# Performance work log

Hardware: AMD Instinct MI355X
Metric: run time of the kernel (lower is better)

Reference implementation:

```python
import jax, jax.numpy as jnp
import numpy as np

TAU = 0.1

def _conv(x, w, padding):
    return jax.lax.conv_general_dilated(
        x, w, window_strides=(1, 1), padding=padding,
        dimension_numbers=("NCHW", "OIHW", "NCHW"))


def _bilinear_border(img, gx, gy):
    # img: (H,W). gx,gy: (H,W) normalized coords in [-1,1].
    # Matches torch grid_sample(mode='bilinear', align_corners=True, padding_mode='border').
    H, W = img.shape
    px = jnp.clip((gx + 1.0) * 0.5 * (W - 1), 0.0, W - 1)  # border: clamp coord
    py = jnp.clip((gy + 1.0) * 0.5 * (H - 1), 0.0, H - 1)
    x0 = jnp.floor(px)
    y0 = jnp.floor(py)
    wx = px - x0
    wy = py - y0
    x0i = x0.astype(jnp.int32)
    y0i = y0.astype(jnp.int32)
    x1i = jnp.minimum(x0i + 1, W - 1)
    y1i = jnp.minimum(y0i + 1, H - 1)
    v00 = img[y0i, x0i]
    v01 = img[y0i, x1i]
    v10 = img[y1i, x0i]
    v11 = img[y1i, x1i]
    top = v00 * (1.0 - wx) + v01 * wx
    bot = v10 * (1.0 - wx) + v11 * wx
    return top * (1.0 - wy) + bot * wy

_sample = jax.vmap(_bilinear_border)  # over flattened B*C axis


def setup_inputs() -> dict:
    key = jax.random.key(0)
    k1, k2, k3, k4 = jax.random.split(key, 4)
    B, C, H, W = 8, 64, 192, 192
    SH = 8
    x = jax.random.normal(k1, (B, C, H, W), dtype=jnp.float32)
    # kaiming_normal * 0.1 scale on first conv
    w1 = jax.random.normal(k2, (SH, C, 3, 3), dtype=jnp.float32) * (np.sqrt(2.0 / (C * 9)) * 0.1)
    # original zero-inits w2; use small random values for a nontrivial reference
    w2 = jax.random.normal(k3, (4 * C, SH, 1, 1), dtype=jnp.float32) * 0.02
    b2 = jax.random.normal(k4, (4 * C,), dtype=jnp.float32) * 0.5
    log_scale = jnp.asarray(np.log(0.1), dtype=jnp.float32)
    return {"x": x, "w1": w1, "w2": w2, "b2": b2, "log_scale": log_scale}


def reference(x, w1, w2, b2, log_scale):
    B, C, H, W = x.shape
    h = jax.nn.gelu(_conv(x, w1, "SAME"), approximate=False)
    coeffs = _conv(h, w2, "VALID") + b2[None, :, None, None]  # (B,4C,H,W)
    coeffs = coeffs.reshape(B, C, 4, H, W)  # channel = c*4 + k, as in torch .view
    a = jax.nn.softplus(coeffs[:, :, 0])
    bx = coeffs[:, :, 1]
    by = coeffs[:, :, 2]
    c = jnp.clip(coeffs[:, :, 3], -5.0, 5.0)
    s = jnp.sqrt(a * TAU + 1e-8).reshape(B * C, H, W)
    dx = (bx * TAU).reshape(B * C, H, W)
    dy = (by * TAU).reshape(B * C, H, W)
    bgx = jnp.broadcast_to(jnp.linspace(-1.0, 1.0, W, dtype=x.dtype)[None, :], (H, W))[None]
    bgy = jnp.broadcast_to(jnp.linspace(-1.0, 1.0, H, dtype=x.dtype)[:, None], (H, W))[None]
    xf = x.reshape(B * C, H, W)
    u_px = _sample(xf, bgx + s + dx, bgy + dy)
    u_nx = _sample(xf, bgx - s + dx, bgy + dy)
    u_py = _sample(xf, bgx + dx, bgy + s + dy)
    u_ny = _sample(xf, bgx + dx, bgy - s + dy)
    evolution = (0.25 * (u_px + u_nx + u_py + u_ny)).reshape(B, C, H, W)
    return jnp.exp(log_scale) * (evolution + TAU * c * x)
```

## Files before the change

kernel.cpp:

```cpp
#include <hip/hip_runtime.h>

#define HH 192
#define WW 192
#define CC 64
#define BB 8
#define SH 8
#define HWSZ (HH*WW)
#define TAU 0.1f

#define AT 16
#define HALO 18
#define PADX 20
#define CCH 8
#define PLANE (HALO*HALO)
#define NELTS (CCH*PLANE)
#define NSLOT 11
#define LDS_C (HALO*PADX)

__global__ __launch_bounds__(256) void conv1_gelu_kernel(
    const float* __restrict__ x, const float* __restrict__ w1, float* __restrict__ h)
{
    __shared__ float tile[CCH][HALO][PADX];
    const int t  = threadIdx.x;
    const int bx = blockIdx.x * AT;
    const int by = blockIdx.y * AT;
    const int b  = blockIdx.z;

    int g_off[NSLOT], l_off[NSLOT];
    bool ok[NSLOT];
#pragma unroll
    for (int i = 0; i < NSLOT; i++) {
        int idx = t + i * 256;
        bool v  = idx < NELTS;
        int cl  = idx / PLANE;
        int rem = idx - cl * PLANE;
        int iy  = rem / HALO;
        int ix  = rem - iy * HALO;
        int gy  = by + iy - 1;
        int gx  = bx + ix - 1;
        bool o  = v && (gy >= 0) && (gy < HH) && (gx >= 0) && (gx < WW);
        ok[i]    = o;
        g_off[i] = o ? (cl * HWSZ + gy * WW + gx) : 0;
        l_off[i] = cl * LDS_C + iy * PADX + ix;
    }

    const int tx = t & 15, ty = t >> 4;

    float acc[SH];
#pragma unroll
    for (int sh = 0; sh < SH; sh++) acc[sh] = 0.f;

    float* tile0 = &tile[0][0][0];

    for (int r = 0; r < CC / CCH; r++) {
        const float* xp = x + ((size_t)(b * CC + r * CCH)) * HWSZ;

        float vals[NSLOT];
#pragma unroll
        for (int i = 0; i < NSLOT; i++) vals[i] = xp[g_off[i]];
#pragma unroll
        for (int i = 0; i < NSLOT; i++) if (!ok[i]) vals[i] = 0.f;

        __syncthreads();
#pragma unroll
        for (int i = 0; i < NSLOT - 1; i++) tile0[l_off[i]] = vals[i];
        if (t < NELTS - (NSLOT - 1) * 256) tile0[l_off[NSLOT - 1]] = vals[NSLOT - 1];
        __syncthreads();

#pragma unroll
        for (int cl = 0; cl < CCH; cl++) {
            float win[3][3];
#pragma unroll
            for (int i = 0; i < 3; i++)
#pragma unroll
                for (int j = 0; j < 3; j++)
                    win[i][j] = tile[cl][ty + i][tx + j];

            const int c = r * CCH + cl;
#pragma unroll
            for (int sh = 0; sh < SH; sh++) {
                const float* ws = w1 + ((size_t)sh * CC + c) * 9;
                float a = acc[sh];
                a = fmaf(win[0][0], ws[0], a);
                a = fmaf(win[0][1], ws[1], a);
                a = fmaf(win[0][2], ws[2], a);
                a = fmaf(win[1][0], ws[3], a);
                a = fmaf(win[1][1], ws[4], a);
                a = fmaf(win[1][2], ws[5], a);
                a = fmaf(win[2][0], ws[6], a);
                a = fmaf(win[2][1], ws[7], a);
                a = fmaf(win[2][2], ws[8], a);
                acc[sh] = a;
            }
        }
    }

    const int pix = (by + ty) * WW + (bx + tx);
    float4 o0, o1;
    float g[SH];
#pragma unroll
    for (int sh = 0; sh < SH; sh++)
        g[sh] = 0.5f * acc[sh] * (1.f + erff(acc[sh] * 0.70710678118654752f));
    o0.x = g[0]; o0.y = g[1]; o0.z = g[2]; o0.w = g[3];
    o1.x = g[4]; o1.y = g[5]; o1.z = g[6]; o1.w = g[7];
    float4* hp = (float4*)&h[((size_t)b * HWSZ + pix) * SH];
    hp[0] = o0;
    hp[1] = o1;
}

__device__ __forceinline__ float sample_x(const float* __restrict__ img,
                                          int r0, int r1, float wy, float px)
{
    px = fminf(fmaxf(px, 0.f), 191.f);
    float x0f = floorf(px);
    float wx  = px - x0f;
    int x0 = (int)x0f;
    int x1 = x0 + ((x0 < WW - 1) ? 1 : 0);
    float v00 = img[r0 + x0], v01 = img[r0 + x1];
    float v10 = img[r1 + x0], v11 = img[r1 + x1];
    float top = fmaf(wx, v01 - v00, v00);
    float bot = fmaf(wx, v11 - v10, v10);
    return fmaf(wy, bot - top, top);
}

__device__ __forceinline__ float sample_y(const float* __restrict__ img,
                                          int x0, int x1, float wx, float py)
{
    py = fminf(fmaxf(py, 0.f), 191.f);
    float y0f = floorf(py);
    float wy  = py - y0f;
    int y0 = (int)y0f;
    int r0 = y0 * WW;
    int r1 = r0 + ((y0 < HH - 1) ? WW : 0);
    float v00 = img[r0 + x0], v01 = img[r0 + x1];
    float v10 = img[r1 + x0], v11 = img[r1 + x1];
    float top = fmaf(wx, v01 - v00, v00);
    float bot = fmaf(wx, v11 - v10, v10);
    return fmaf(wy, bot - top, top);
}

#define TILES_PER_PLANE 144
#define NPLANES (BB*CC)

__global__ __launch_bounds__(256) void coeff_sample_kernel(
    const float* __restrict__ x, const float* __restrict__ hbuf,
    const float* __restrict__ w2, const float* __restrict__ b2,
    const float* __restrict__ log_scale, float* __restrict__ out)
{
    const int li = blockIdx.x;
    const int rr = li & 7;
    const int m  = li >> 3;
    const int q  = m / TILES_PER_PLANE;
    const int tt = m - q * TILES_PER_PLANE;
    const int bc = (q << 3) | rr;
    const int tyb = tt / 12, txb = tt - tyb * 12;

    const int t  = threadIdx.x;
    const int tx = t & 15;
    const int ty = t >> 4;
    const int xo = txb * 16 + tx;
    const int y  = tyb * 16 + ty;
    const int c  = bc & 63;
    const int pix = y * WW + xo;

    const float4* hp4 = (const float4*)&hbuf[((size_t)(bc >> 6) * HWSZ + pix) * SH];
    float4 h0 = hp4[0], h1 = hp4[1];
    float hk[SH] = {h0.x, h0.y, h0.z, h0.w, h1.x, h1.y, h1.z, h1.w};

    const int c4 = c * 4;
    float coeff[4];
#pragma unroll
    for (int j = 0; j < 4; j++) {
        const float* wr = w2 + (size_t)(c4 + j) * SH;
        float s = b2[c4 + j];
#pragma unroll
        for (int k = 0; k < SH; k++) s = fmaf(hk[k], wr[k], s);
        coeff[j] = s;
    }

    float z  = coeff[0];
    float a  = fmaxf(z, 0.f) + __logf(1.f + __expf(-fabsf(z)));
    float s  = __builtin_amdgcn_sqrtf(fmaf(a, TAU, 1e-8f));
    float dx = coeff[1] * TAU;
    float dy = coeff[2] * TAU;
    float cc = fminf(fmaxf(coeff[3], -5.f), 5.f);

    const float* img = x + (size_t)bc * HWSZ;
    const float px0 = (float)xo + dx * 95.5f;
    const float py0 = (float)y  + dy * 95.5f;
    const float sp  = s * 95.5f;

    float u;
    {
        float py  = fminf(fmaxf(py0, 0.f), 191.f);
        float y0f = floorf(py);
        float wy  = py - y0f;
        int y0 = (int)y0f;
        int r0 = y0 * WW;
        int r1 = r0 + ((y0 < HH - 1) ? WW : 0);
        u = sample_x(img, r0, r1, wy, px0 + sp)
          + sample_x(img, r0, r1, wy, px0 - sp);
    }
    {
        float px  = fminf(fmaxf(px0, 0.f), 191.f);
        float x0f = floorf(px);
        float wx  = px - x0f;
        int x0 = (int)x0f;
        int x1 = x0 + ((x0 < WW - 1) ? 1 : 0);
        u += sample_y(img, x0, x1, wx, py0 + sp)
           + sample_y(img, x0, x1, wx, py0 - sp);
    }

    float xv    = img[pix];
    float scale = __expf(log_scale[0]);
    out[(size_t)bc * HWSZ + pix] = scale * fmaf(0.25f, u, TAU * cc * xv);
}

extern "C" void kernel_launch(void* const* d_in, const int* in_sizes, int n_in,
                              void* d_out, int out_size, void* d_ws, size_t ws_size,
                              hipStream_t stream)
{
    const float* x   = (const float*)d_in[0];
    const float* w1  = (const float*)d_in[1];
    const float* w2  = (const float*)d_in[2];
    const float* b2  = (const float*)d_in[3];
    const float* ls  = (const float*)d_in[4];
    float* out = (float*)d_out;
    float* h   = (float*)d_ws;

    dim3 blk(256);
    dim3 g1(WW / AT, HH / AT, BB);
    conv1_gelu_kernel<<<g1, blk, 0, stream>>>(x, w1, h);

    coeff_sample_kernel<<<dim3(NPLANES * TILES_PER_PLANE), blk, 0, stream>>>(
        x, h, w2, b2, ls, out);
}
```

Baseline: 324.1 us.

## Double-buffer conv1 LDS tiles and remap grid to interleave batches

The conv1 kernel now uses two LDS tile buffers. It issues global loads for the next 8-channel chunk before computing on the current one, which hides load latency and drops one barrier per iteration. The grid is flattened so that consecutive blocks cover different batch images at the same spatial tile, changing how work spreads across CUs. LDS row padding grows from 20 to 24, and total LDS per block roughly doubles, which may lower occupancy.

```diff
diff --git a/kernel.cpp b/kernel.cpp
--- a/kernel.cpp
+++ b/kernel.cpp
@@ -10,7 +10,7 @@
 
 #define AT 16
 #define HALO 18
-#define PADX 20
+#define PADX 24
 #define CCH 8
 #define PLANE (HALO*HALO)
 #define NELTS (CCH*PLANE)
@@ -20,25 +20,29 @@
 __global__ __launch_bounds__(256) void conv1_gelu_kernel(
     const float* __restrict__ x, const float* __restrict__ w1, float* __restrict__ h)
 {
-    __shared__ float tile[CCH][HALO][PADX];
+    __shared__ float tile[2][CCH][HALO][PADX];
     const int t  = threadIdx.x;
-    const int bx = blockIdx.x * AT;
-    const int by = blockIdx.y * AT;
-    const int b  = blockIdx.z;
+
+    const int li  = blockIdx.x;
+    const int b   = li & 7;
+    const int m   = li >> 3;
+    const int tyb = m / 12, txb = m - tyb * 12;
+    const int bx  = txb * AT, by = tyb * AT;
 
     int g_off[NSLOT], l_off[NSLOT];
-    bool ok[NSLOT];
+    bool ok[NSLOT], inr[NSLOT];
 #pragma unroll
     for (int i = 0; i < NSLOT; i++) {
         int idx = t + i * 256;
         bool v  = idx < NELTS;
-        int cl  = idx / PLANE;
+        int cl  = v ? (idx / PLANE) : 0;
         int rem = idx - cl * PLANE;
         int iy  = rem / HALO;
         int ix  = rem - iy * HALO;
         int gy  = by + iy - 1;
         int gx  = bx + ix - 1;
         bool o  = v && (gy >= 0) && (gy < HH) && (gx >= 0) && (gx < WW);
+        inr[i]   = v;
         ok[i]    = o;
         g_off[i] = o ? (cl * HWSZ + gy * WW + gx) : 0;
         l_off[i] = cl * LDS_C + iy * PADX + ix;
@@ -50,22 +54,32 @@
 #pragma unroll
     for (int sh = 0; sh < SH; sh++) acc[sh] = 0.f;
 
-    float* tile0 = &tile[0][0][0];
+    const float* xp0 = x + (size_t)b * CC * HWSZ;
+    float* tbuf0 = &tile[0][0][0][0];
+    float* tbuf1 = &tile[1][0][0][0];
+
+    {
+        float vals[NSLOT];
+#pragma unroll
+        for (int i = 0; i < NSLOT; i++) vals[i] = xp0[g_off[i]];
+#pragma unroll
+        for (int i = 0; i < NSLOT; i++) if (!ok[i]) vals[i] = 0.f;
+#pragma unroll
+        for (int i = 0; i < NSLOT; i++) if (inr[i]) tbuf0[l_off[i]] = vals[i];
+    }
 
     for (int r = 0; r < CC / CCH; r++) {
-        const float* xp = x + ((size_t)(b * CC + r * CCH)) * HWSZ;
-
-        float vals[NSLOT];
-#pragma unroll
-        for (int i = 0; i < NSLOT; i++) vals[i] = xp[g_off[i]];
-#pragma unroll
-        for (int i = 0; i < NSLOT; i++) if (!ok[i]) vals[i] = 0.f;
-
         __syncthreads();
-#pragma unroll
-        for (int i = 0; i < NSLOT - 1; i++) tile0[l_off[i]] = vals[i];
-        if (t < NELTS - (NSLOT - 1) * 256) tile0[l_off[NSLOT - 1]] = vals[NSLOT - 1];
-        __syncthreads();
+        const int cur = r & 1;
+        float* tcur = cur ? tbuf1 : tbuf0;
+        float* tnxt = cur ? tbuf0 : tbuf1;
+
+        float nxt[NSLOT];
+        if (r < CC / CCH - 1) {
+            const float* xp = xp0 + (size_t)((r + 1) * CCH) * HWSZ;
+#pragma unroll
+            for (int i = 0; i < NSLOT; i++) nxt[i] = xp[g_off[i]];
+        }
 
 #pragma unroll
         for (int cl = 0; cl < CCH; cl++) {
@@ -74,7 +88,7 @@
             for (int i = 0; i < 3; i++)
 #pragma unroll
                 for (int j = 0; j < 3; j++)
-                    win[i][j] = tile[cl][ty + i][tx + j];
+                    win[i][j] = tcur[cl * LDS_C + (ty + i) * PADX + (tx + j)];
 
             const int c = r * CCH + cl;
 #pragma unroll
@@ -93,14 +107,21 @@
                 acc[sh] = a;
             }
         }
+
+        if (r < CC / CCH - 1) {
+#pragma unroll
+            for (int i = 0; i < NSLOT; i++) if (!ok[i]) nxt[i] = 0.f;
+#pragma unroll
+            for (int i = 0; i < NSLOT; i++) if (inr[i]) tnxt[l_off[i]] = nxt[i];
+        }
     }
 
     const int pix = (by + ty) * WW + (bx + tx);
-    float4 o0, o1;
     float g[SH];
 #pragma unroll
     for (int sh = 0; sh < SH; sh++)
         g[sh] = 0.5f * acc[sh] * (1.f + erff(acc[sh] * 0.70710678118654752f));
+    float4 o0, o1;
     o0.x = g[0]; o0.y = g[1]; o0.z = g[2]; o0.w = g[3];
     o1.x = g[4]; o1.y = g[5]; o1.z = g[6]; o1.w = g[7];
     float4* hp = (float4*)&h[((size_t)b * HWSZ + pix) * SH];
@@ -229,8 +250,7 @@
     float* h   = (float*)d_ws;
 
     dim3 blk(256);
-    dim3 g1(WW / AT, HH / AT, BB);
-    conv1_gelu_kernel<<<g1, blk, 0, stream>>>(x, w1, h);
+    conv1_gelu_kernel<<<dim3(12 * 12 * BB), blk, 0, stream>>>(x, w1, h);
 
     coeff_sample_kernel<<<dim3(NPLANES * TILES_PER_PLANE), blk, 0, stream>>>(
         x, h, w2, b2, ls, out);
```

After: 393.2 us. +21.3%, slower.

## Replace LDS-tiled conv1 with direct global loads and interior/border split

Applied to the files above, without the earlier changes.

The conv1+GELU kernel drops its shared-memory halo tile and the __syncthreads barriers, and instead reads each 3x3 neighbourhood straight from global memory, relying on L1/L2 caches to supply reuse between neighbouring threads. Interior tiles use unmasked fixed-offset loads, while border tiles use clamped offsets with zero masks. The grid is flattened so the batch index is the fastest-varying block index, which groups blocks that share spatial tiles. This trades explicit LDS reuse for roughly nine cached global loads per pixel per channel, which may be limited by L1 bandwidth.

```diff
diff --git a/kernel.cpp b/kernel.cpp
--- a/kernel.cpp
+++ b/kernel.cpp
@@ -8,99 +8,83 @@
 #define HWSZ (HH*WW)
 #define TAU 0.1f
 
-#define AT 16
-#define HALO 18
-#define PADX 20
-#define CCH 8
-#define PLANE (HALO*HALO)
-#define NELTS (CCH*PLANE)
-#define NSLOT 11
-#define LDS_C (HALO*PADX)
-
 __global__ __launch_bounds__(256) void conv1_gelu_kernel(
     const float* __restrict__ x, const float* __restrict__ w1, float* __restrict__ h)
 {
-    __shared__ float tile[CCH][HALO][PADX];
+    const int li  = blockIdx.x;
+    const int b   = li & 7;
+    const int m   = li >> 3;
+    const int tyb = m / 12, txb = m - tyb * 12;
+
     const int t  = threadIdx.x;
-    const int bx = blockIdx.x * AT;
-    const int by = blockIdx.y * AT;
-    const int b  = blockIdx.z;
-
-    int g_off[NSLOT], l_off[NSLOT];
-    bool ok[NSLOT];
-#pragma unroll
-    for (int i = 0; i < NSLOT; i++) {
-        int idx = t + i * 256;
-        bool v  = idx < NELTS;
-        int cl  = idx / PLANE;
-        int rem = idx - cl * PLANE;
-        int iy  = rem / HALO;
-        int ix  = rem - iy * HALO;
-        int gy  = by + iy - 1;
-        int gx  = bx + ix - 1;
-        bool o  = v && (gy >= 0) && (gy < HH) && (gx >= 0) && (gx < WW);
-        ok[i]    = o;
-        g_off[i] = o ? (cl * HWSZ + gy * WW + gx) : 0;
-        l_off[i] = cl * LDS_C + iy * PADX + ix;
-    }
-
     const int tx = t & 15, ty = t >> 4;
+    const int xo = txb * 16 + tx;
+    const int yo = tyb * 16 + ty;
+    const int pix = yo * WW + xo;
+
+    const float* xb = x + (size_t)b * CC * HWSZ;
 
     float acc[SH];
 #pragma unroll
     for (int sh = 0; sh < SH; sh++) acc[sh] = 0.f;
 
-    float* tile0 = &tile[0][0][0];
-
-    for (int r = 0; r < CC / CCH; r++) {
-        const float* xp = x + ((size_t)(b * CC + r * CCH)) * HWSZ;
-
-        float vals[NSLOT];
-#pragma unroll
-        for (int i = 0; i < NSLOT; i++) vals[i] = xp[g_off[i]];
-#pragma unroll
-        for (int i = 0; i < NSLOT; i++) if (!ok[i]) vals[i] = 0.f;
-
-        __syncthreads();
-#pragma unroll
-        for (int i = 0; i < NSLOT - 1; i++) tile0[l_off[i]] = vals[i];
-        if (t < NELTS - (NSLOT - 1) * 256) tile0[l_off[NSLOT - 1]] = vals[NSLOT - 1];
-        __syncthreads();
-
-#pragma unroll
-        for (int cl = 0; cl < CCH; cl++) {
-            float win[3][3];
-#pragma unroll
-            for (int i = 0; i < 3; i++)
-#pragma unroll
-                for (int j = 0; j < 3; j++)
-                    win[i][j] = tile[cl][ty + i][tx + j];
-
-            const int c = r * CCH + cl;
+    const bool border = (txb == 0) | (txb == 11) | (tyb == 0) | (tyb == 11);
+
+    if (!border) {
+        const float* p = xb + pix;
+#pragma unroll 2
+        for (int c = 0; c < CC; c++) {
+            const float* pc = p + (size_t)c * HWSZ;
+            float v[9];
+            v[0] = pc[-WW - 1]; v[1] = pc[-WW]; v[2] = pc[-WW + 1];
+            v[3] = pc[-1];      v[4] = pc[0];   v[5] = pc[1];
+            v[6] = pc[WW - 1];  v[7] = pc[WW];  v[8] = pc[WW + 1];
+            const float* wc = w1 + c * 9;
 #pragma unroll
             for (int sh = 0; sh < SH; sh++) {
-                const float* ws = w1 + ((size_t)sh * CC + c) * 9;
+                const float* ws = wc + (size_t)sh * CC * 9;
                 float a = acc[sh];
-                a = fmaf(win[0][0], ws[0], a);
-                a = fmaf(win[0][1], ws[1], a);
-                a = fmaf(win[0][2], ws[2], a);
-                a = fmaf(win[1][0], ws[3], a);
-                a = fmaf(win[1][1], ws[4], a);
-                a = fmaf(win[1][2], ws[5], a);
-                a = fmaf(win[2][0], ws[6], a);
-                a = fmaf(win[2][1], ws[7], a);
-                a = fmaf(win[2][2], ws[8], a);
+#pragma unroll
+                for (int k = 0; k < 9; k++) a = fmaf(v[k], ws[k], a);
                 acc[sh] = a;
             }
         }
-    }
-
-    const int pix = (by + ty) * WW + (bx + tx);
-    float4 o0, o1;
+    } else {
+        const int ym1 = max(yo - 1, 0), yp1 = min(yo + 1, HH - 1);
+        const int xm1 = max(xo - 1, 0), xp1 = min(xo + 1, WW - 1);
+        const int r0 = ym1 * WW, r1 = yo * WW, r2 = yp1 * WW;
+        const bool vy0 = yo > 0, vy2 = yo < HH - 1, vx0 = xo > 0, vx2 = xo < WW - 1;
+        int  o[9]  = {r0 + xm1, r0 + xo, r0 + xp1,
+                      r1 + xm1, r1 + xo, r1 + xp1,
+                      r2 + xm1, r2 + xo, r2 + xp1};
+        bool mk[9] = {vy0 && vx0, vy0, vy0 && vx2,
+                      vx0,        true, vx2,
+                      vy2 && vx0, vy2, vy2 && vx2};
+#pragma unroll 2
+        for (int c = 0; c < CC; c++) {
+            const float* pc = xb + (size_t)c * HWSZ;
+            float v[9];
+#pragma unroll
+            for (int k = 0; k < 9; k++) v[k] = pc[o[k]];
+#pragma unroll
+            for (int k = 0; k < 9; k++) if (!mk[k]) v[k] = 0.f;
+            const float* wc = w1 + c * 9;
+#pragma unroll
+            for (int sh = 0; sh < SH; sh++) {
+                const float* ws = wc + (size_t)sh * CC * 9;
+                float a = acc[sh];
+#pragma unroll
+                for (int k = 0; k < 9; k++) a = fmaf(v[k], ws[k], a);
+                acc[sh] = a;
+            }
+        }
+    }
+
     float g[SH];
 #pragma unroll
     for (int sh = 0; sh < SH; sh++)
         g[sh] = 0.5f * acc[sh] * (1.f + erff(acc[sh] * 0.70710678118654752f));
+    float4 o0, o1;
     o0.x = g[0]; o0.y = g[1]; o0.z = g[2]; o0.w = g[3];
     o1.x = g[4]; o1.y = g[5]; o1.z = g[6]; o1.w = g[7];
     float4* hp = (float4*)&h[((size_t)b * HWSZ + pix) * SH];
@@ -229,8 +213,7 @@
     float* h   = (float*)d_ws;
 
     dim3 blk(256);
-    dim3 g1(WW / AT, HH / AT, BB);
-    conv1_gelu_kernel<<<g1, blk, 0, stream>>>(x, w1, h);
+    conv1_gelu_kernel<<<dim3(12 * 12 * BB), blk, 0, stream>>>(x, w1, h);
 
     coeff_sample_kernel<<<dim3(NPLANES * TILES_PER_PLANE), blk, 0, stream>>>(
         x, h, w2, b2, ls, out);
```

Result: faster. 289.3 us (-10.8%).
